# Kernel tuning notes

Hardware: AMD Instinct MI355X
Metric: run time of the kernel (lower is better)

Reference implementation:

```python
import jax, jax.numpy as jnp
import numpy as np

N_HEADS = 16
N_EMBED = 1024
HEAD_SIZE = 64


def setup_inputs() -> dict:
    key = jax.random.key(0)
    ks = jax.random.split(key, 6)
    B, T, C = 2, 2048, N_EMBED
    x = jax.random.normal(ks[0], (B, T, C), dtype=jnp.float32)
    s = 1.0 / np.sqrt(C)
    Wq = jax.random.normal(ks[1], (N_HEADS, C, HEAD_SIZE), dtype=jnp.float32) * s
    Wk = jax.random.normal(ks[2], (N_HEADS, C, HEAD_SIZE), dtype=jnp.float32) * s
    Wv = jax.random.normal(ks[3], (N_HEADS, C, HEAD_SIZE), dtype=jnp.float32) * s
    Wo = jax.random.normal(ks[4], (C, C), dtype=jnp.float32) * s
    bo = jax.random.normal(ks[5], (C,), dtype=jnp.float32) * 0.01
    return {"x": x, "Wq": Wq, "Wk": Wk, "Wv": Wv, "Wo": Wo, "bo": bo}


def reference(x, Wq, Wk, Wv, Wo, bo):
    B, T, C = x.shape
    # per-head projections: [B, H, T, D]
    q = jnp.einsum('btc,hcd->bhtd', x, Wq)
    k = jnp.einsum('btc,hcd->bhtd', x, Wk)
    v = jnp.einsum('btc,hcd->bhtd', x, Wv)
    # NOTE: original scales by n_embed**0.5 (C), not head_size**0.5
    scores = jnp.einsum('bhtd,bhsd->bhts', q, k) / jnp.sqrt(jnp.float32(C))
    causal = jnp.tril(jnp.ones((T, T), dtype=bool))
    scores = jnp.where(causal, scores, -jnp.inf)
    wei = jax.nn.softmax(scores, axis=-1)
    out = jnp.einsum('bhts,bhsd->bhtd', wei, v)  # [B, H, T, D]
    out = out.transpose(0, 2, 1, 3).reshape(B, T, C)  # concat heads
    return out @ Wo.T + bo
```

## Files before the change

### kernel.cpp

```cpp
#include <hip/hip_runtime.h>


#define Bsz 2
#define Tsz 2048
#define Cdim 1024
#define Hn 16
#define Dh 64

typedef short bf16x8 __attribute__((ext_vector_type(8)));
typedef float f32x4 __attribute__((ext_vector_type(4)));
typedef unsigned short u16;

#define MFMA(a, b, c) __builtin_amdgcn_mfma_f32_16x16x32_bf16(a, b, c, 0, 0, 0)
#define NEGINF (-__builtin_inff())
#define EXP2(x) __builtin_amdgcn_exp2f(x)

#define GLD16(g, l)                                                            \
  __builtin_amdgcn_global_load_lds((const __attribute__((address_space(1))) void*)(g), \
                                   (__attribute__((address_space(3))) void*)(l), 16, 0, 0)

__device__ __forceinline__ u16 f2bf(float f) {
  unsigned u = __builtin_bit_cast(unsigned, f);
  unsigned r = 0x7fffu + ((u >> 16) & 1u);
  return (u16)((u + r) >> 16);
}

__device__ __forceinline__ unsigned cvtpk(float lo, float hi) {
  unsigned r;
  asm("v_cvt_pk_bf16_f32 %0, %1, %2" : "=v"(r) : "v"(lo), "v"(hi));
  return r;
}

__global__ __launch_bounds__(256) void k_cast_x(const float* __restrict__ x,
                                                u16* __restrict__ xb, int n4) {
  int i = blockIdx.x * 256 + threadIdx.x;
  if (i >= n4) return;
  float4 v = reinterpret_cast<const float4*>(x)[i];
  ushort4 o;
  o.x = f2bf(v.x); o.y = f2bf(v.y); o.z = f2bf(v.z); o.w = f2bf(v.w);
  reinterpret_cast<ushort4*>(xb)[i] = o;
}

__global__ __launch_bounds__(256) void k_cast_w(const float* __restrict__ Wq,
                                                const float* __restrict__ Wk,
                                                const float* __restrict__ Wv,
                                                u16* __restrict__ wt) {
  __shared__ u16 tile[64][68];
  const int mh = blockIdx.y;
  const int m = mh >> 4, h = mh & 15;
  const float* src = (m == 0 ? Wq : m == 1 ? Wk : Wv) + (size_t)h * Cdim * Dh;
  const int c0 = blockIdx.x * 64;
  const int tid = threadIdx.x;
  const int cc = tid >> 4, d4 = (tid & 15) * 4;
#pragma unroll
  for (int i = 0; i < 4; ++i) {
    int c = i * 16 + cc;
    float4 v = *(const float4*)(src + (size_t)(c0 + c) * Dh + d4);
    tile[d4 + 0][c] = f2bf(v.x);
    tile[d4 + 1][c] = f2bf(v.y);
    tile[d4 + 2][c] = f2bf(v.z);
    tile[d4 + 3][c] = f2bf(v.w);
  }
  __syncthreads();
  const int c4 = (tid & 15) * 4, dd = tid >> 4;
#pragma unroll
  for (int i = 0; i < 4; ++i) {
    int d = i * 16 + dd;
    ushort4 o;
    o.x = tile[d][c4]; o.y = tile[d][c4 + 1];
    o.z = tile[d][c4 + 2]; o.w = tile[d][c4 + 3];
    *(ushort4*)(wt + (size_t)(mh * 64 + d) * Cdim + c0 + c4) = o;
  }
}

__global__ __launch_bounds__(256) void k_gemm_qkv(const u16* __restrict__ xb,
                                                  const u16* __restrict__ wt,
                                                  u16* __restrict__ qb,
                                                  u16* __restrict__ kb,
                                                  u16* __restrict__ vtb) {
  __shared__ __align__(16) u16 As[3][4096], Bs[3][4096];
  const int tid = threadIdx.x, lane = tid & 63, wid = tid >> 6;
  const int cl = lane & 15, kg = lane >> 4;
  const int row0 = blockIdx.y * 128, col0 = blockIdx.x * 128;
  const int wrow = (wid >> 1) * 64, wcol = (wid & 1) * 64;
  f32x4 acc[4][4] = {};
  const int csrc = ((lane & 3) ^ ((lane >> 3) & 3)) * 8;
  const u16* a_src = xb + (size_t)(row0 + 32 * wid + (lane >> 2)) * Cdim + csrc;
  const u16* b_src = wt + (size_t)(col0 + 32 * wid + (lane >> 2)) * Cdim + csrc;

  auto stage = [&](int buf, int ke) {
    u16* Ad = &As[buf][1024 * wid];
    u16* Bd = &Bs[buf][1024 * wid];
    GLD16(a_src + ke, Ad);
    GLD16(a_src + 16 * Cdim + ke, Ad + 512);
    GLD16(b_src + ke, Bd);
    GLD16(b_src + 16 * Cdim + ke, Bd + 512);
  };

  const int rdswz = (kg ^ ((cl >> 1) & 3)) * 8;

  stage(0, 0);
  stage(1, 32);
  stage(2, 64);
  for (int kk = 0; kk < 32; ++kk) {
    if (kk < 30)
      asm volatile("s_waitcnt vmcnt(8)" ::: "memory");
    else if (kk == 30)
      asm volatile("s_waitcnt vmcnt(4)" ::: "memory");
    else
      asm volatile("s_waitcnt vmcnt(0)" ::: "memory");
    __builtin_amdgcn_s_barrier();
    const int cur = kk % 3;
    const u16* ar = &As[cur][(wrow + cl) * 32 + rdswz];
    const u16* br = &Bs[cur][(wcol + cl) * 32 + rdswz];
    bf16x8 af[4], bfr[4];
#pragma unroll
    for (int mi = 0; mi < 4; ++mi) af[mi] = *(const bf16x8*)(ar + mi * 512);
#pragma unroll
    for (int ni = 0; ni < 4; ++ni) bfr[ni] = *(const bf16x8*)(br + ni * 512);
#pragma unroll
    for (int mi = 0; mi < 4; ++mi)
#pragma unroll
      for (int ni = 0; ni < 4; ++ni)
        acc[mi][ni] = MFMA(af[mi], bfr[ni], acc[mi][ni]);
    __builtin_amdgcn_s_barrier();
    if (kk + 3 < 32) stage(cur, (kk + 3) * 32);
  }
#pragma unroll
  for (int mi = 0; mi < 4; ++mi) {
#pragma unroll
    for (int ni = 0; ni < 4; ++ni) {
      int n = col0 + wcol + ni * 16 + cl;
      int m = n >> 10, h = (n >> 6) & 15, d = n & 63;
#pragma unroll
      for (int j = 0; j < 4; ++j) {
        int r = row0 + wrow + mi * 16 + kg * 4 + j;
        int b = r >> 11, t = r & 2047;
        float av = acc[mi][ni][j];
        if (m == 0) av *= 0.04508422f;
        u16 v = f2bf(av);
        size_t bh = (size_t)(b * Hn + h);
        if (m == 0)
          qb[(bh * Tsz + t) * Dh + d] = v;
        else if (m == 1)
          kb[(bh * Tsz + t) * Dh + d] = v;
        else
          vtb[(bh * Dh + d) * Tsz + t] = v;
      }
    }
  }
}

__global__ __launch_bounds__(256, 2) void k_attn(const u16* __restrict__ qb,
                                                 const u16* __restrict__ kb,
                                                 const u16* __restrict__ vtb,
                                                 u16* __restrict__ ob) {
  __shared__ __align__(16) u16 KV[2][8192];
  __shared__ __align__(16) u16 Plds[4][2][1024];
  const int lane = threadIdx.x & 63, wid = threadIdx.x >> 6;
  const int cl = lane & 15, kg = lane >> 4;
  const int bid = blockIdx.x;
  const int kdec = bid >> 3;
  const int p = (bid & 7) + ((kdec >> 4) << 3);
  const int tp = kdec & 15;
  const int h = p & 15, b = p >> 4;
  const int tA = tp, tB = 31 - tp;
  const int qrA = tA * 64 + wid * 16;
  const int qrB = tB * 64 + wid * 16;
  const size_t bh = (size_t)(b * Hn + h);
  const u16* Qp = qb + bh * Tsz * Dh;
  const u16* Kp = kb + bh * Tsz * Dh;
  const u16* Vp = vtb + bh * Dh * Tsz;

  const u16* pk_src[2];
  const u16* pv_src[2];
#pragma unroll
  for (int c = 0; c < 2; ++c) {
    int lo = c * 4096 + wid * 1024 + lane * 16;
    int r = lo >> 7, cb = lo & 127;
    int cbs = cb ^ ((r & 7) << 4);
    pk_src[c] = Kp + r * Dh + (cbs >> 1);
    pv_src[c] = Vp + (size_t)r * Tsz + (cbs >> 1);
  }

  auto stage = [&](int buf, int kt) {
    GLD16(pk_src[0] + kt * 4096, &KV[buf][(wid * 1024) >> 1]);
    GLD16(pk_src[1] + kt * 4096, &KV[buf][(4096 + wid * 1024) >> 1]);
    GLD16(pv_src[0] + kt * 64, &KV[buf][(8192 + wid * 1024) >> 1]);
    GLD16(pv_src[1] + kt * 64, &KV[buf][(12288 + wid * 1024) >> 1]);
  };

  bf16x8 qaA0 = *(const bf16x8*)(Qp + (size_t)(qrA + cl) * Dh + kg * 8);
  bf16x8 qaA1 = *(const bf16x8*)(Qp + (size_t)(qrA + cl) * Dh + 32 + kg * 8);
  bf16x8 qaB0 = *(const bf16x8*)(Qp + (size_t)(qrB + cl) * Dh + kg * 8);
  bf16x8 qaB1 = *(const bf16x8*)(Qp + (size_t)(qrB + cl) * Dh + 32 + kg * 8);

  f32x4 oA[4] = {}, oB[4] = {};
  float mA = NEGINF, lA = 0.f, mB = NEGINF, lB = 0.f;

  char* pbA = (char*)&Plds[wid][0][0];
  char* pbB = (char*)&Plds[wid][1][0];
  const int rdoff0 = ((cl << 7) + (kg << 4)) ^ ((cl & 7) << 4);
  const int rdoff1 = ((cl << 7) + 64 + (kg << 4)) ^ ((cl & 7) << 4);
  const int rowoff = wid * 16;
  const int swz0 = (kg * 16) ^ ((cl & 7) << 4);
  const int swz1 = (kg * 16 + 64) ^ ((cl & 7) << 4);

  auto sm_pv = [&](f32x4 s[4], float& m, float& l, f32x4 o[4],
                   const bf16x8 vf[8], char* pb, bool mask) {
    if (mask) {
#pragma unroll
      for (int nt = 0; nt < 4; ++nt)
#pragma unroll
        for (int j = 0; j < 4; ++j)
          if (nt * 16 + kg * 4 + j > rowoff + cl) s[nt][j] = NEGINF;
    }
    float tm = fmaxf(fmaxf(fmaxf(s[0][0], s[0][1]), fmaxf(s[0][2], s[0][3])),
                     fmaxf(fmaxf(s[1][0], s[1][1]), fmaxf(s[1][2], s[1][3])));
    tm = fmaxf(tm, fmaxf(fmaxf(fmaxf(s[2][0], s[2][1]), fmaxf(s[2][2], s[2][3])),
                         fmaxf(fmaxf(s[3][0], s[3][1]), fmaxf(s[3][2], s[3][3]))));
    if (!__all(tm <= m + 8.0f)) {
      tm = fmaxf(tm, __shfl_xor(tm, 16));
      tm = fmaxf(tm, __shfl_xor(tm, 32));
      float mnew = fmaxf(m, tm);
      float corr = EXP2(m - mnew);
      m = mnew;
      l *= corr;
      float c0 = __shfl(corr, kg * 4 + 0);
      float c1 = __shfl(corr, kg * 4 + 1);
      float c2 = __shfl(corr, kg * 4 + 2);
      float c3 = __shfl(corr, kg * 4 + 3);
#pragma unroll
      for (int dt = 0; dt < 4; ++dt) {
        o[dt][0] *= c0; o[dt][1] *= c1; o[dt][2] *= c2; o[dt][3] *= c3;
      }
    }
    float rs = 0.f;
#pragma unroll
    for (int nt = 0; nt < 4; ++nt)
#pragma unroll
      for (int j = 0; j < 4; ++j) {
        float pv = EXP2(s[nt][j] - m);
        s[nt][j] = pv;
        rs += pv;
      }
    l += rs;
#pragma unroll
    for (int nt = 0; nt < 4; ++nt) {
      uint2 pk;
      pk.x = cvtpk(s[nt][0], s[nt][1]);
      pk.y = cvtpk(s[nt][2], s[nt][3]);
      int waddr = ((cl << 7) + (nt << 5) + (kg << 3)) ^ ((cl & 7) << 4);
      *(uint2*)(pb + waddr) = pk;
    }
    bf16x8 pa0 = *(const bf16x8*)(pb + rdoff0);
    bf16x8 pa1 = *(const bf16x8*)(pb + rdoff1);
    __builtin_amdgcn_s_setprio(1);
#pragma unroll
    for (int dt = 0; dt < 4; ++dt) {
      o[dt] = MFMA(pa0, vf[dt * 2], o[dt]);
      o[dt] = MFMA(pa1, vf[dt * 2 + 1], o[dt]);
    }
    __builtin_amdgcn_s_setprio(0);
  };

  const int ntot = tB + 1;
  stage(0, 0);
  __syncthreads();
  int cur = 0;
  for (int t = 0; t < ntot; ++t) {
    if (t + 1 < ntot) stage(cur ^ 1, t + 1);
    char* kvb = (char*)&KV[cur][0];
    bf16x8 ka[8];
#pragma unroll
    for (int nt = 0; nt < 4; ++nt) {
      int rbase = (nt * 16 + cl) << 7;
      ka[nt * 2] = *(const bf16x8*)(kvb + rbase + swz0);
      ka[nt * 2 + 1] = *(const bf16x8*)(kvb + rbase + swz1);
    }
    f32x4 sB[4];
    __builtin_amdgcn_s_setprio(1);
#pragma unroll
    for (int nt = 0; nt < 4; ++nt) {
      f32x4 z = {};
      z = MFMA(ka[nt * 2], qaB0, z);
      z = MFMA(ka[nt * 2 + 1], qaB1, z);
      sB[nt] = z;
    }
    __builtin_amdgcn_s_setprio(0);
    f32x4 sA[4];
    const bool actA = (t <= tA);
    if (actA) {
      __builtin_amdgcn_s_setprio(1);
#pragma unroll
      for (int nt = 0; nt < 4; ++nt) {
        f32x4 z = {};
        z = MFMA(ka[nt * 2], qaA0, z);
        z = MFMA(ka[nt * 2 + 1], qaA1, z);
        sA[nt] = z;
      }
      __builtin_amdgcn_s_setprio(0);
    }
    bf16x8 vf[8];
#pragma unroll
    for (int dt = 0; dt < 4; ++dt) {
      int rbase = 8192 + ((dt * 16 + cl) << 7);
      vf[dt * 2] = *(const bf16x8*)(kvb + rbase + swz0);
      vf[dt * 2 + 1] = *(const bf16x8*)(kvb + rbase + swz1);
    }
    if (actA) sm_pv(sA, mA, lA, oA, vf, pbA, t == tA);
    sm_pv(sB, mB, lB, oB, vf, pbB, t == tB);
    __syncthreads();
    cur ^= 1;
  }

  lA += __shfl_xor(lA, 16); lA += __shfl_xor(lA, 32);
  lB += __shfl_xor(lB, 16); lB += __shfl_xor(lB, 32);
  float iA0 = 1.f / __shfl(lA, kg * 4 + 0), iA1 = 1.f / __shfl(lA, kg * 4 + 1);
  float iA2 = 1.f / __shfl(lA, kg * 4 + 2), iA3 = 1.f / __shfl(lA, kg * 4 + 3);
  float iB0 = 1.f / __shfl(lB, kg * 4 + 0), iB1 = 1.f / __shfl(lB, kg * 4 + 1);
  float iB2 = 1.f / __shfl(lB, kg * 4 + 2), iB3 = 1.f / __shfl(lB, kg * 4 + 3);
  float invA[4] = {iA0, iA1, iA2, iA3};
  float invB[4] = {iB0, iB1, iB2, iB3};
#pragma unroll
  for (int dt = 0; dt < 4; ++dt)
#pragma unroll
    for (int j = 0; j < 4; ++j) {
      int ta = qrA + kg * 4 + j;
      int tb = qrB + kg * 4 + j;
      ob[(size_t)(b * Tsz + ta) * Cdim + h * Dh + dt * 16 + cl] = f2bf(oA[dt][j] * invA[j]);
      ob[(size_t)(b * Tsz + tb) * Cdim + h * Dh + dt * 16 + cl] = f2bf(oB[dt][j] * invB[j]);
    }
}

__global__ __launch_bounds__(256) void k_gemm_out(const u16* __restrict__ ob,
                                                  const u16* __restrict__ wob,
                                                  const float* __restrict__ bo,
                                                  float* __restrict__ out) {
  __shared__ __align__(16) u16 As[3][4096], Bs[3][2048];
  const int tid = threadIdx.x, lane = tid & 63, wid = tid >> 6;
  const int cl = lane & 15, kg = lane >> 4;
  const int row0 = blockIdx.y * 128, col0 = blockIdx.x * 64;
  const int wrow = (wid >> 1) * 64, wcol = (wid & 1) * 32;
  f32x4 acc[4][2] = {};
  const int csrc = ((lane & 3) ^ ((lane >> 3) & 3)) * 8;
  const u16* a_src = ob + (size_t)(row0 + 32 * wid + (lane >> 2)) * Cdim + csrc;
  const u16* b_src = wob + (size_t)(col0 + 16 * wid + (lane >> 2)) * Cdim + csrc;

  auto stage = [&](int buf, int ke) {
    u16* Ad = &As[buf][1024 * wid];
    u16* Bd = &Bs[buf][512 * wid];
    GLD16(a_src + ke, Ad);
    GLD16(a_src + 16 * Cdim + ke, Ad + 512);
    GLD16(b_src + ke, Bd);
  };

  const int rdswz = (kg ^ ((cl >> 1) & 3)) * 8;

  stage(0, 0);
  stage(1, 32);
  stage(2, 64);
  for (int kk = 0; kk < 32; ++kk) {
    if (kk < 30)
      asm volatile("s_waitcnt vmcnt(6)" ::: "memory");
    else if (kk == 30)
      asm volatile("s_waitcnt vmcnt(3)" ::: "memory");
    else
      asm volatile("s_waitcnt vmcnt(0)" ::: "memory");
    __builtin_amdgcn_s_barrier();
    const int cur = kk % 3;
    const u16* ar = &As[cur][(wrow + cl) * 32 + rdswz];
    const u16* br = &Bs[cur][(wcol + cl) * 32 + rdswz];
    bf16x8 af[4], bfr[2];
#pragma unroll
    for (int mi = 0; mi < 4; ++mi) af[mi] = *(const bf16x8*)(ar + mi * 512);
#pragma unroll
    for (int ni = 0; ni < 2; ++ni) bfr[ni] = *(const bf16x8*)(br + ni * 512);
#pragma unroll
    for (int mi = 0; mi < 4; ++mi)
#pragma unroll
      for (int ni = 0; ni < 2; ++ni)
        acc[mi][ni] = MFMA(af[mi], bfr[ni], acc[mi][ni]);
    __builtin_amdgcn_s_barrier();
    if (kk + 3 < 32) stage(cur, (kk + 3) * 32);
  }
#pragma unroll
  for (int mi = 0; mi < 4; ++mi) {
#pragma unroll
    for (int ni = 0; ni < 2; ++ni) {
      int n = col0 + wcol + ni * 16 + cl;
      float bias = bo[n];
#pragma unroll
      for (int j = 0; j < 4; ++j) {
        int r = row0 + wrow + mi * 16 + kg * 4 + j;
        out[(size_t)r * Cdim + n] = acc[mi][ni][j] + bias;
      }
    }
  }
}

extern "C" void kernel_launch(void* const* d_in, const int* in_sizes, int n_in,
                              void* d_out, int out_size, void* d_ws, size_t ws_size,
                              hipStream_t stream) {
  (void)in_sizes; (void)n_in; (void)out_size; (void)ws_size;
  const float* x = (const float*)d_in[0];
  const float* Wq = (const float*)d_in[1];
  const float* Wk = (const float*)d_in[2];
  const float* Wv = (const float*)d_in[3];
  const float* Wo = (const float*)d_in[4];
  const float* bo = (const float*)d_in[5];
  float* out = (float*)d_out;
  char* ws = (char*)d_ws;
  u16* xb = (u16*)(ws);
  u16* wt = (u16*)(ws + (8u << 20));
  u16* wob = (u16*)(ws + (14u << 20));
  u16* qb = (u16*)(ws + (16u << 20));
  u16* kb = (u16*)(ws + (24u << 20));
  u16* vtb = (u16*)(ws + (32u << 20));
  u16* ob = (u16*)(ws + (40u << 20));

  k_cast_x<<<4096, 256, 0, stream>>>(x, xb, Bsz * Tsz * Cdim / 4);
  k_cast_x<<<1024, 256, 0, stream>>>(Wo, wob, Cdim * Cdim / 4);
  k_cast_w<<<dim3(16, 48), 256, 0, stream>>>(Wq, Wk, Wv, wt);
  k_gemm_qkv<<<dim3(24, 32), 256, 0, stream>>>(xb, wt, qb, kb, vtb);
  k_attn<<<512, 256, 0, stream>>>(qb, kb, vtb, ob);
  k_gemm_out<<<dim3(16, 32), 256, 0, stream>>>(ob, wob, bo, out);
}
```

Before: 116.6 us.

## Split paired-tile attention blocks into one query tile per block, longest first

```diff
diff --git a/kernel.cpp b/kernel.cpp
--- a/kernel.cpp
+++ b/kernel.cpp
@@ -151,22 +151,19 @@
   }
 }
 
-__global__ __launch_bounds__(256, 2) void k_attn(const u16* __restrict__ qb,
+__global__ __launch_bounds__(256, 4) void k_attn(const u16* __restrict__ qb,
                                                  const u16* __restrict__ kb,
                                                  const u16* __restrict__ vtb,
                                                  u16* __restrict__ ob) {
   __shared__ __align__(16) u16 KV[2][8192];
-  __shared__ __align__(16) u16 Plds[4][2][1024];
+  __shared__ __align__(16) u16 Plds[4][1024];
   const int lane = threadIdx.x & 63, wid = threadIdx.x >> 6;
   const int cl = lane & 15, kg = lane >> 4;
-  const int bid = blockIdx.x;
-  const int kdec = bid >> 3;
-  const int p = (bid & 7) + ((kdec >> 4) << 3);
-  const int tp = kdec & 15;
+  const int s = blockIdx.x >> 3;
+  const int t = 31 - (s >> 2);
+  const int p = (blockIdx.x & 7) + 8 * (s & 3);
   const int h = p & 15, b = p >> 4;
-  const int tA = tp, tB = 31 - tp;
-  const int qrA = tA * 64 + wid * 16;
-  const int qrB = tB * 64 + wid * 16;
+  const int qr = t * 64 + wid * 16;
   const size_t bh = (size_t)(b * Hn + h);
   const u16* Qp = qb + bh * Tsz * Dh;
   const u16* Kp = kb + bh * Tsz * Dh;
@@ -190,35 +187,60 @@
     GLD16(pv_src[1] + kt * 64, &KV[buf][(12288 + wid * 1024) >> 1]);
   };
 
-  bf16x8 qaA0 = *(const bf16x8*)(Qp + (size_t)(qrA + cl) * Dh + kg * 8);
-  bf16x8 qaA1 = *(const bf16x8*)(Qp + (size_t)(qrA + cl) * Dh + 32 + kg * 8);
-  bf16x8 qaB0 = *(const bf16x8*)(Qp + (size_t)(qrB + cl) * Dh + kg * 8);
-  bf16x8 qaB1 = *(const bf16x8*)(Qp + (size_t)(qrB + cl) * Dh + 32 + kg * 8);
-
-  f32x4 oA[4] = {}, oB[4] = {};
-  float mA = NEGINF, lA = 0.f, mB = NEGINF, lB = 0.f;
-
-  char* pbA = (char*)&Plds[wid][0][0];
-  char* pbB = (char*)&Plds[wid][1][0];
+  bf16x8 qa0 = *(const bf16x8*)(Qp + (size_t)(qr + cl) * Dh + kg * 8);
+  bf16x8 qa1 = *(const bf16x8*)(Qp + (size_t)(qr + cl) * Dh + 32 + kg * 8);
+
+  f32x4 o[4] = {};
+  float m = NEGINF, l = 0.f;
+
+  char* pb = (char*)&Plds[wid][0];
   const int rdoff0 = ((cl << 7) + (kg << 4)) ^ ((cl & 7) << 4);
   const int rdoff1 = ((cl << 7) + 64 + (kg << 4)) ^ ((cl & 7) << 4);
   const int rowoff = wid * 16;
   const int swz0 = (kg * 16) ^ ((cl & 7) << 4);
   const int swz1 = (kg * 16 + 64) ^ ((cl & 7) << 4);
 
-  auto sm_pv = [&](f32x4 s[4], float& m, float& l, f32x4 o[4],
-                   const bf16x8 vf[8], char* pb, bool mask) {
-    if (mask) {
+  stage(0, 0);
+  __syncthreads();
+  int cur = 0;
+  for (int kt = 0; kt <= t; ++kt) {
+    if (kt < t) stage(cur ^ 1, kt + 1);
+    char* kvb = (char*)&KV[cur][0];
+    bf16x8 ka[8];
+#pragma unroll
+    for (int nt = 0; nt < 4; ++nt) {
+      int rbase = (nt * 16 + cl) << 7;
+      ka[nt * 2] = *(const bf16x8*)(kvb + rbase + swz0);
+      ka[nt * 2 + 1] = *(const bf16x8*)(kvb + rbase + swz1);
+    }
+    f32x4 sv[4];
+    __builtin_amdgcn_s_setprio(1);
+#pragma unroll
+    for (int nt = 0; nt < 4; ++nt) {
+      f32x4 z = {};
+      z = MFMA(ka[nt * 2], qa0, z);
+      z = MFMA(ka[nt * 2 + 1], qa1, z);
+      sv[nt] = z;
+    }
+    __builtin_amdgcn_s_setprio(0);
+    bf16x8 vf[8];
+#pragma unroll
+    for (int dt = 0; dt < 4; ++dt) {
+      int rbase = 8192 + ((dt * 16 + cl) << 7);
+      vf[dt * 2] = *(const bf16x8*)(kvb + rbase + swz0);
+      vf[dt * 2 + 1] = *(const bf16x8*)(kvb + rbase + swz1);
+    }
+    if (kt == t) {
 #pragma unroll
       for (int nt = 0; nt < 4; ++nt)
 #pragma unroll
         for (int j = 0; j < 4; ++j)
-          if (nt * 16 + kg * 4 + j > rowoff + cl) s[nt][j] = NEGINF;
-    }
-    float tm = fmaxf(fmaxf(fmaxf(s[0][0], s[0][1]), fmaxf(s[0][2], s[0][3])),
-                     fmaxf(fmaxf(s[1][0], s[1][1]), fmaxf(s[1][2], s[1][3])));
-    tm = fmaxf(tm, fmaxf(fmaxf(fmaxf(s[2][0], s[2][1]), fmaxf(s[2][2], s[2][3])),
-                         fmaxf(fmaxf(s[3][0], s[3][1]), fmaxf(s[3][2], s[3][3]))));
+          if (nt * 16 + kg * 4 + j > rowoff + cl) sv[nt][j] = NEGINF;
+    }
+    float tm = fmaxf(fmaxf(fmaxf(sv[0][0], sv[0][1]), fmaxf(sv[0][2], sv[0][3])),
+                     fmaxf(fmaxf(sv[1][0], sv[1][1]), fmaxf(sv[1][2], sv[1][3])));
+    tm = fmaxf(tm, fmaxf(fmaxf(fmaxf(sv[2][0], sv[2][1]), fmaxf(sv[2][2], sv[2][3])),
+                         fmaxf(fmaxf(sv[3][0], sv[3][1]), fmaxf(sv[3][2], sv[3][3]))));
     if (!__all(tm <= m + 8.0f)) {
       tm = fmaxf(tm, __shfl_xor(tm, 16));
       tm = fmaxf(tm, __shfl_xor(tm, 32));
@@ -240,16 +262,16 @@
     for (int nt = 0; nt < 4; ++nt)
 #pragma unroll
       for (int j = 0; j < 4; ++j) {
-        float pv = EXP2(s[nt][j] - m);
-        s[nt][j] = pv;
+        float pv = EXP2(sv[nt][j] - m);
+        sv[nt][j] = pv;
         rs += pv;
       }
     l += rs;
 #pragma unroll
     for (int nt = 0; nt < 4; ++nt) {
       uint2 pk;
-      pk.x = cvtpk(s[nt][0], s[nt][1]);
-      pk.y = cvtpk(s[nt][2], s[nt][3]);
+      pk.x = cvtpk(sv[nt][0], sv[nt][1]);
+      pk.y = cvtpk(sv[nt][2], sv[nt][3]);
       int waddr = ((cl << 7) + (nt << 5) + (kg << 3)) ^ ((cl & 7) << 4);
       *(uint2*)(pb + waddr) = pk;
     }
@@ -262,74 +284,21 @@
       o[dt] = MFMA(pa1, vf[dt * 2 + 1], o[dt]);
     }
     __builtin_amdgcn_s_setprio(0);
-  };
-
-  const int ntot = tB + 1;
-  stage(0, 0);
-  __syncthreads();
-  int cur = 0;
-  for (int t = 0; t < ntot; ++t) {
-    if (t + 1 < ntot) stage(cur ^ 1, t + 1);
-    char* kvb = (char*)&KV[cur][0];
-    bf16x8 ka[8];
-#pragma unroll
-    for (int nt = 0; nt < 4; ++nt) {
-      int rbase = (nt * 16 + cl) << 7;
-      ka[nt * 2] = *(const bf16x8*)(kvb + rbase + swz0);
-      ka[nt * 2 + 1] = *(const bf16x8*)(kvb + rbase + swz1);
-    }
-    f32x4 sB[4];
-    __builtin_amdgcn_s_setprio(1);
-#pragma unroll
-    for (int nt = 0; nt < 4; ++nt) {
-      f32x4 z = {};
-      z = MFMA(ka[nt * 2], qaB0, z);
-      z = MFMA(ka[nt * 2 + 1], qaB1, z);
-      sB[nt] = z;
-    }
-    __builtin_amdgcn_s_setprio(0);
-    f32x4 sA[4];
-    const bool actA = (t <= tA);
-    if (actA) {
-      __builtin_amdgcn_s_setprio(1);
-#pragma unroll
-      for (int nt = 0; nt < 4; ++nt) {
-        f32x4 z = {};
-        z = MFMA(ka[nt * 2], qaA0, z);
-        z = MFMA(ka[nt * 2 + 1], qaA1, z);
-        sA[nt] = z;
-      }
-      __builtin_amdgcn_s_setprio(0);
-    }
-    bf16x8 vf[8];
-#pragma unroll
-    for (int dt = 0; dt < 4; ++dt) {
-      int rbase = 8192 + ((dt * 16 + cl) << 7);
-      vf[dt * 2] = *(const bf16x8*)(kvb + rbase + swz0);
-      vf[dt * 2 + 1] = *(const bf16x8*)(kvb + rbase + swz1);
-    }
-    if (actA) sm_pv(sA, mA, lA, oA, vf, pbA, t == tA);
-    sm_pv(sB, mB, lB, oB, vf, pbB, t == tB);
     __syncthreads();
     cur ^= 1;
   }
 
-  lA += __shfl_xor(lA, 16); lA += __shfl_xor(lA, 32);
-  lB += __shfl_xor(lB, 16); lB += __shfl_xor(lB, 32);
-  float iA0 = 1.f / __shfl(lA, kg * 4 + 0), iA1 = 1.f / __shfl(lA, kg * 4 + 1);
-  float iA2 = 1.f / __shfl(lA, kg * 4 + 2), iA3 = 1.f / __shfl(lA, kg * 4 + 3);
-  float iB0 = 1.f / __shfl(lB, kg * 4 + 0), iB1 = 1.f / __shfl(lB, kg * 4 + 1);
-  float iB2 = 1.f / __shfl(lB, kg * 4 + 2), iB3 = 1.f / __shfl(lB, kg * 4 + 3);
-  float invA[4] = {iA0, iA1, iA2, iA3};
-  float invB[4] = {iB0, iB1, iB2, iB3};
+  l += __shfl_xor(l, 16);
+  l += __shfl_xor(l, 32);
+  float i0 = 1.f / __shfl(l, kg * 4 + 0), i1 = 1.f / __shfl(l, kg * 4 + 1);
+  float i2 = 1.f / __shfl(l, kg * 4 + 2), i3 = 1.f / __shfl(l, kg * 4 + 3);
+  float inv[4] = {i0, i1, i2, i3};
 #pragma unroll
   for (int dt = 0; dt < 4; ++dt)
 #pragma unroll
     for (int j = 0; j < 4; ++j) {
-      int ta = qrA + kg * 4 + j;
-      int tb = qrB + kg * 4 + j;
-      ob[(size_t)(b * Tsz + ta) * Cdim + h * Dh + dt * 16 + cl] = f2bf(oA[dt][j] * invA[j]);
-      ob[(size_t)(b * Tsz + tb) * Cdim + h * Dh + dt * 16 + cl] = f2bf(oB[dt][j] * invB[j]);
+      int tr = qr + kg * 4 + j;
+      ob[(size_t)(b * Tsz + tr) * Cdim + h * Dh + dt * 16 + cl] = f2bf(o[dt][j] * inv[j]);
     }
 }
 
@@ -423,6 +392,6 @@
   k_cast_x<<<1024, 256, 0, stream>>>(Wo, wob, Cdim * Cdim / 4);
   k_cast_w<<<dim3(16, 48), 256, 0, stream>>>(Wq, Wk, Wv, wt);
   k_gemm_qkv<<<dim3(24, 32), 256, 0, stream>>>(xb, wt, qb, kb, vtb);
-  k_attn<<<512, 256, 0, stream>>>(qb, kb, vtb, ob);
+  k_attn<<<1024, 256, 0, stream>>>(qb, kb, vtb, ob);
   k_gemm_out<<<dim3(16, 32), 256, 0, stream>>>(ob, wob, bo, out);
 }
```

After: 112.5 us. -3.5%, faster.
